# Performance work log

Hardware: AMD Instinct MI355X
Metric: run time of the kernel (lower is better)

## Reference

```python
import jax, jax.numpy as jnp
import numpy as np
import math

B, C_IN, N_SEL, N_DROP, HEADS = 4, 128, 1024, 1024, 4
Q_OUT = K_OUT = V_OUT = 256
N = N_SEL + N_DROP


def setup_inputs() -> dict:
    key = jax.random.key(0)
    ks = jax.random.split(key, 8)
    pcd_up = jax.random.normal(ks[0], (B, C_IN, N), jnp.float32)
    points_select = jax.random.normal(ks[1], (B, C_IN, N_SEL), jnp.float32)
    points_drop = jax.random.normal(ks[2], (B, C_IN, N_DROP), jnp.float32)
    # per-batch permutation of [0, N) split into select/drop halves (collision-free scatter)
    perms = jax.vmap(lambda k: jax.random.permutation(k, N))(jax.random.split(ks[3], B))
    idx_select = perms[:, None, :N_SEL].astype(jnp.int32)
    idx_drop = perms[:, None, N_SEL:].astype(jnp.int32)
    scale = 1.0 / math.sqrt(C_IN)
    Wq = jax.random.normal(ks[4], (Q_OUT, C_IN), jnp.float32) * scale
    Wk = jax.random.normal(ks[5], (K_OUT, C_IN), jnp.float32) * scale
    Wv = jax.random.normal(ks[6], (V_OUT, C_IN), jnp.float32) * scale
    Wskip = jax.random.normal(ks[7], (V_OUT, C_IN), jnp.float32) * scale
    return {"pcd_up": pcd_up, "points_select": points_select, "points_drop": points_drop,
            "idx_select": idx_select, "idx_drop": idx_drop,
            "Wq": Wq, "Wk": Wk, "Wv": Wv, "Wskip": Wskip}


def _concat_by_idx(a, b, idx_a, idx_b):
    # scatter columns of concat([a,b]) to positions given by concat([idx_a, idx_b])
    src = jnp.concatenate([a, b], axis=-1)            # (B, C, N)
    idx = jnp.concatenate([idx_a, idx_b], axis=-1)[:, 0, :]  # (B, N)
    return jax.vmap(lambda s, i: jnp.zeros_like(s).at[:, i].set(s))(src, idx)


def reference(pcd_up, points_select, points_drop, idx_select, idx_drop, Wq, Wk, Wv, Wskip):
    b, _, n = pcd_up.shape
    x = _concat_by_idx(points_select, points_drop, idx_select, idx_drop)  # (B, C_in, N)
    # 1x1 convs (no bias) == channel matmuls, then split heads: (B, H, D, N)
    q = jnp.einsum('oc,bcn->bon', Wq, x).reshape(b, HEADS, Q_OUT // HEADS, n)
    k = jnp.einsum('oc,bcn->bon', Wk, x).reshape(b, HEADS, K_OUT // HEADS, n)
    v = jnp.einsum('oc,bcn->bon', Wv, x).reshape(b, HEADS, V_OUT // HEADS, n)
    energy = jnp.einsum('bhdn,bhdm->bhnm', q, k)      # (B, H, N, N)
    attn = jax.nn.softmax(energy / math.sqrt(Q_OUT // HEADS), axis=-1)
    out = jnp.einsum('bhnm,bhdm->bhnd', attn, v)      # (B, H, N, Dv)
    out = out.transpose(0, 2, 1, 3).reshape(b, n, V_OUT).transpose(0, 2, 1)  # (B, V_out, N)
    skip = jnp.einsum('oc,bcn->bon', Wskip, pcd_up)   # (B, V_out, N)
    return skip + out
```

## Files before the change

### kernel.cpp

```cpp
#include <hip/hip_runtime.h>
#include <hip/hip_bf16.h>
#include <math.h>

#define B_    4
#define C_IN_ 128
#define N_    2048
#define NSEL_ 1024
#define H_    4
#define KS_   2

typedef __bf16 bf16;
typedef __bf16 bf16x2 __attribute__((ext_vector_type(2)));
typedef __bf16 bf16x4 __attribute__((ext_vector_type(4)));
typedef __bf16 bf16x8 __attribute__((ext_vector_type(8)));
typedef float  f32x4  __attribute__((ext_vector_type(4)));

__global__ __launch_bounds__(256) void prep_kernel(
    const int* __restrict__ isel, const int* __restrict__ idrp,
    const float* __restrict__ Wq, const float* __restrict__ Wk,
    const float* __restrict__ Wv, const float* __restrict__ Ws,
    int* __restrict__ inv, bf16* __restrict__ Wbf)
{
    const int blk = blockIdx.x;
    if (blk < 128) {
        int e = blk * 256 + threadIdx.x;
        int which = e >> 13, idx = e & 8191;
        const float* Wx = (which == 0) ? Wq : (which == 1) ? Wk
                        : (which == 2) ? Wv : Ws;
        float4 v = *(const float4*)(Wx + (size_t)idx * 4);
        bf16x4 o; o[0] = (bf16)v.x; o[1] = (bf16)v.y; o[2] = (bf16)v.z; o[3] = (bf16)v.w;
        *(bf16x4*)(Wbf + (size_t)which * 32768 + (size_t)idx * 4) = o;
    } else {
        int g = (blk - 128) * 256 + threadIdx.x;
        int b = g >> 11, j = g & (N_ - 1);
        int pos = (j < NSEL_) ? isel[b * NSEL_ + j] : idrp[b * NSEL_ + (j - NSEL_)];
        inv[b * N_ + (pos & (N_ - 1))] = j;
    }
}

#define XSTR 136

__global__ __launch_bounds__(256) void qkv_mfma_kernel(
    const float* __restrict__ pcd, const float* __restrict__ sel,
    const float* __restrict__ drop, const bf16* __restrict__ Wbf,
    bf16* __restrict__ qT, bf16* __restrict__ kTt, bf16* __restrict__ vTt)
{
    const int ntile = blockIdx.x;
    const int which = blockIdx.y >> 1;
    const int rh    = blockIdx.y & 1;
    const int b     = blockIdx.z;
    const int tid   = threadIdx.x;
    const int w     = tid >> 6;
    const int lane  = tid & 63;
    const int quad  = lane >> 4;
    const int lc    = lane & 15;
    const int n0    = ntile * 64;

    __shared__ __align__(16) bf16 xT[64 * XSTR];

    const float* srcp; int rstride;
    if (ntile < 16) { srcp = sel  + (size_t)b * C_IN_ * NSEL_ + n0;           rstride = NSEL_; }
    else            { srcp = drop + (size_t)b * C_IN_ * NSEL_ + (n0 - NSEL_); rstride = NSEL_; }

    #pragma unroll
    for (int k = 0; k < 4; ++k) {
        int e  = tid + k * 256;
        int cp = e >> 4, nq = e & 15;
        int c0 = cp * 2;
        float4 v0 = *(const float4*)(srcp + (size_t)c0 * rstride + nq * 4);
        float4 v1 = *(const float4*)(srcp + (size_t)(c0 + 1) * rstride + nq * 4);
        int cc = c0 ^ ((nq & 3) << 3);
        float a0[4] = {v0.x, v0.y, v0.z, v0.w};
        float a1[4] = {v1.x, v1.y, v1.z, v1.w};
        #pragma unroll
        for (int i = 0; i < 4; ++i) {
            int n = nq * 4 + i;
            bf16x2 t; t[0] = (bf16)a0[i]; t[1] = (bf16)a1[i];
            *(bf16x2*)&xT[n * XSTR + cc] = t;
        }
    }
    __syncthreads();

    const bf16* wbase = Wbf + (size_t)which * 256 * 128;
    const int rbase = rh * 128 + w * 32;

    f32x4 acc[8];
    #pragma unroll
    for (int i = 0; i < 8; ++i) acc[i] = (f32x4){0.f, 0.f, 0.f, 0.f};

    #pragma unroll
    for (int kq = 0; kq < 4; ++kq) {
        bf16x8 wf[2], xA[4];
        #pragma unroll
        for (int ot = 0; ot < 2; ++ot)
            wf[ot] = *(const bf16x8*)(wbase + (size_t)(rbase + ot * 16 + lc) * 128 + kq * 32 + quad * 8);
        #pragma unroll
        for (int nt = 0; nt < 4; ++nt) {
            int row = nt * 16 + lc;
            int col = (kq * 32 + quad * 8) ^ (((row >> 2) & 3) << 3);
            xA[nt] = *(const bf16x8*)&xT[row * XSTR + col];
        }
        if (which <= 1) {
            #pragma unroll
            for (int nt = 0; nt < 4; ++nt)
                #pragma unroll
                for (int ot = 0; ot < 2; ++ot)
                    acc[nt * 2 + ot] = __builtin_amdgcn_mfma_f32_16x16x32_bf16(xA[nt], wf[ot], acc[nt * 2 + ot], 0, 0, 0);
        } else {
            #pragma unroll
            for (int ot = 0; ot < 2; ++ot)
                #pragma unroll
                for (int nt = 0; nt < 4; ++nt)
                    acc[ot * 4 + nt] = __builtin_amdgcn_mfma_f32_16x16x32_bf16(wf[ot], xA[nt], acc[ot * 4 + nt], 0, 0, 0);
        }
    }

    if (which <= 1) {
        #pragma unroll
        for (int nt = 0; nt < 4; ++nt) {
            #pragma unroll
            for (int ot = 0; ot < 2; ++ot) {
                #pragma unroll
                for (int r = 0; r < 4; ++r) {
                    int n    = n0 + nt * 16 + quad * 4 + r;
                    int rloc = nt * 16 + quad * 4 + r;
                    int o256 = rbase + ot * 16 + lc;
                    int h = o256 >> 6, d = o256 & 63;
                    float val = acc[nt * 2 + ot][r];
                    if (which == 0)
                        qT[((size_t)(b * H_ + h) * N_ + n) * 64 + d] = (bf16)(val * 0.125f);
                    else
                        kTt[(((size_t)(b * H_ + h) * 32 + ntile) << 12) | (rloc << 6) | d] = (bf16)val;
                }
            }
        }
    } else {
        #pragma unroll
        for (int ot = 0; ot < 2; ++ot) {
            #pragma unroll
            for (int r = 0; r < 4; ++r) {
                int o256 = rbase + ot * 16 + quad * 4 + r;
                int h = o256 >> 6, dv = o256 & 63;
                bf16x4 pk;
                #pragma unroll
                for (int nt = 0; nt < 4; ++nt) pk[nt] = (bf16)acc[ot * 4 + nt][r];
                *(bf16x4*)(vTt + ((((size_t)(b * H_ + h) * 32 + ntile) << 12) | (dv << 6) | (lc * 4))) = pk;
            }
        }
    }
}

#define PSTR 72
#define KVSTR 72

__global__ __launch_bounds__(256, 2) void attn_kernel(
    const bf16* __restrict__ qT, const bf16* __restrict__ kTt,
    const bf16* __restrict__ vTt, bf16* __restrict__ Opart,
    float* __restrict__ S_ws)
{
    const int id    = blockIdx.x;
    const int bh    = (id & 7) + 8 * ((id >> 3) & 1);
    const int qb    = (id >> 4) & 15;
    const int c     = id >> 8;
    const int b     = bh >> 2;
    const int h     = bh & 3;
    const int tid   = threadIdx.x;
    const int w     = tid >> 6;
    const int lane  = tid & 63;
    const int quad  = lane >> 4;
    const int lc    = lane & 15;
    const int n0    = qb * 128 + w * 32;

    __shared__ __align__(16) bf16 sK[2][64 * KVSTR];
    __shared__ __align__(16) bf16 sV[2][64 * KVSTR];
    __shared__ __align__(16) bf16 p_lds[4 * 16 * PSTR];
    bf16* pw = &p_lds[w * 16 * PSTR];

    bf16x8 aq[2][2];
    #pragma unroll
    for (int t = 0; t < 2; ++t) {
        const bf16* qp = qT + ((size_t)bh * N_ + n0 + t * 16 + lc) * 64 + quad * 8;
        aq[t][0] = *(const bf16x8*)(qp);
        aq[t][1] = *(const bf16x8*)(qp + 32);
    }

    const bf16* kbase = kTt + (((size_t)bh * 32 + c * 16) << 12);
    const bf16* vbase = vTt + (((size_t)bh * 32 + c * 16) << 12);

    const int l0 = (tid >> 3) * KVSTR + (tid & 7) * 8;
    const int l1 = ((tid >> 3) + 32) * KVSTR + (tid & 7) * 8;

    bf16x8 ldK0 = *(const bf16x8*)(kbase + tid * 8);
    bf16x8 ldK1 = *(const bf16x8*)(kbase + 2048 + tid * 8);
    bf16x8 ldV0 = *(const bf16x8*)(vbase + tid * 8);
    bf16x8 ldV1 = *(const bf16x8*)(vbase + 2048 + tid * 8);

    f32x4 accO[2][4];
    #pragma unroll
    for (int t = 0; t < 2; ++t)
        #pragma unroll
        for (int i = 0; i < 4; ++i) accO[t][i] = (f32x4){0.f, 0.f, 0.f, 0.f};
    float psum[2][4] = {{0.f,0.f,0.f,0.f},{0.f,0.f,0.f,0.f}};

    for (int s = 0; s < 16; ++s) {
        const int buf = s & 1;
        *(bf16x8*)&sK[buf][l0] = ldK0;
        *(bf16x8*)&sK[buf][l1] = ldK1;
        *(bf16x8*)&sV[buf][l0] = ldV0;
        *(bf16x8*)&sV[buf][l1] = ldV1;
        __syncthreads();

        if (s < 15) {
            const bf16* kg = kbase + ((size_t)(s + 1) << 12);
            const bf16* vg = vbase + ((size_t)(s + 1) << 12);
            ldK0 = *(const bf16x8*)(kg + tid * 8);
            ldK1 = *(const bf16x8*)(kg + 2048 + tid * 8);
            ldV0 = *(const bf16x8*)(vg + tid * 8);
            ldV1 = *(const bf16x8*)(vg + 2048 + tid * 8);
        }

        bf16x8 kf[4][2], vf[4][2];
        #pragma unroll
        for (int mt = 0; mt < 4; ++mt) {
            const int rb = (mt * 16 + lc) * KVSTR + quad * 8;
            kf[mt][0] = *(const bf16x8*)&sK[buf][rb];
            kf[mt][1] = *(const bf16x8*)&sK[buf][rb + 32];
            vf[mt][0] = *(const bf16x8*)&sV[buf][rb];
            vf[mt][1] = *(const bf16x8*)&sV[buf][rb + 32];
        }

        #pragma unroll
        for (int t = 0; t < 2; ++t) {
            f32x4 accS[4];
            #pragma unroll
            for (int mt = 0; mt < 4; ++mt) {
                f32x4 z = (f32x4){0.f, 0.f, 0.f, 0.f};
                z = __builtin_amdgcn_mfma_f32_16x16x32_bf16(aq[t][0], kf[mt][0], z, 0, 0, 0);
                z = __builtin_amdgcn_mfma_f32_16x16x32_bf16(aq[t][1], kf[mt][1], z, 0, 0, 0);
                accS[mt] = z;
            }
            #pragma unroll
            for (int r = 0; r < 4; ++r) {
                float sum = 0.f;
                #pragma unroll
                for (int mt = 0; mt < 4; ++mt) {
                    float p = __expf(accS[mt][r]);
                    accS[mt][r] = p;
                    sum += p;
                }
                psum[t][r] += sum;
            }
            #pragma unroll
            for (int r = 0; r < 4; ++r) {
                bf16x4 pk;
                #pragma unroll
                for (int mt = 0; mt < 4; ++mt) pk[mt] = (bf16)accS[mt][r];
                *(bf16x4*)&pw[(quad * 4 + r) * PSTR + lc * 4] = pk;
            }
            bf16x8 ap0 = *(const bf16x8*)(&pw[lc * PSTR + quad * 8]);
            bf16x8 ap1 = *(const bf16x8*)(&pw[lc * PSTR + 32 + quad * 8]);
            #pragma unroll
            for (int dvt = 0; dvt < 4; ++dvt) {
                accO[t][dvt] = __builtin_amdgcn_mfma_f32_16x16x32_bf16(ap0, vf[dvt][0], accO[t][dvt], 0, 0, 0);
                accO[t][dvt] = __builtin_amdgcn_mfma_f32_16x16x32_bf16(ap1, vf[dvt][1], accO[t][dvt], 0, 0, 0);
            }
        }
    }

    #pragma unroll
    for (int t = 0; t < 2; ++t) {
        float inv[4];
        #pragma unroll
        for (int r = 0; r < 4; ++r) {
            float s = psum[t][r];
            #pragma unroll
            for (int off = 1; off < 16; off <<= 1)
                s += __shfl_xor(s, off, 64);
            inv[r] = 1.f / s;
            int n = n0 + t * 16 + quad * 4 + r;
            if (lc == 0)
                S_ws[((size_t)(c * B_ + b) * H_ + h) * N_ + n] = s;
        }
        #pragma unroll
        for (int r = 0; r < 4; ++r) {
            int n = n0 + t * 16 + quad * 4 + r;
            #pragma unroll
            for (int dvt = 0; dvt < 4; ++dvt) {
                int o = h * 64 + dvt * 16 + lc;
                Opart[((size_t)(c * B_ + b) * N_ + n) * 256 + o] = (bf16)(accO[t][dvt][r] * inv[r]);
            }
        }
    }
}

__global__ __launch_bounds__(256) void scatter_kernel(
    const bf16* __restrict__ Opart, const float* __restrict__ S_ws,
    const int* __restrict__ inv, const float* __restrict__ pcd,
    const bf16* __restrict__ Wbf, float* __restrict__ out)
{
    const int ptile = blockIdx.x;
    const int og    = blockIdx.y;
    const int b     = blockIdx.z;
    const int tid   = threadIdx.x;
    const int w     = tid >> 6;
    const int lane  = tid & 63;
    const int quad  = lane >> 4;
    const int lc    = lane & 15;
    const int p0    = ptile * 64;

    __shared__ __align__(16) bf16 xT[64 * XSTR];
    __shared__ __align__(16) bf16 lds[64 * 72];
    __shared__ float wls[KS_][64];
    __shared__ int   jrow[64];

    const float* srcp = pcd + (size_t)b * C_IN_ * N_ + p0;
    #pragma unroll
    for (int k = 0; k < 4; ++k) {
        int e  = tid + k * 256;
        int cp = e >> 4, nq = e & 15;
        int c0 = cp * 2;
        float4 v0 = *(const float4*)(srcp + (size_t)c0 * N_ + nq * 4);
        float4 v1 = *(const float4*)(srcp + (size_t)(c0 + 1) * N_ + nq * 4);
        int cc = c0 ^ ((nq & 3) << 3);
        float a0[4] = {v0.x, v0.y, v0.z, v0.w};
        float a1[4] = {v1.x, v1.y, v1.z, v1.w};
        #pragma unroll
        for (int i = 0; i < 4; ++i) {
            int n = nq * 4 + i;
            bf16x2 t; t[0] = (bf16)a0[i]; t[1] = (bf16)a1[i];
            *(bf16x2*)&xT[n * XSTR + cc] = t;
        }
    }
    if (tid < 64) {
        int row = tid;
        int j = inv[b * N_ + p0 + row] & (N_ - 1);
        jrow[row] = j;
        float sv[KS_]; float denom = 0.f;
        #pragma unroll
        for (int c = 0; c < KS_; ++c) {
            sv[c] = S_ws[((size_t)(c * B_ + b) * H_ + og) * N_ + j];
            denom += sv[c];
        }
        float idn = 1.f / denom;
        #pragma unroll
        for (int c = 0; c < KS_; ++c) wls[c][row] = sv[c] * idn;
    }
    __syncthreads();

    const bf16* wbase = Wbf + (size_t)3 * 256 * 128 + (size_t)(og * 64 + w * 16) * 128;
    f32x4 acc[4];
    #pragma unroll
    for (int i = 0; i < 4; ++i) acc[i] = (f32x4){0.f, 0.f, 0.f, 0.f};
    #pragma unroll
    for (int kq = 0; kq < 4; ++kq) {
        bf16x8 A = *(const bf16x8*)(wbase + (size_t)lc * 128 + kq * 32 + quad * 8);
        #pragma unroll
        for (int nt = 0; nt < 4; ++nt) {
            int row = nt * 16 + lc;
            int col = (kq * 32 + quad * 8) ^ (((row >> 2) & 3) << 3);
            bf16x8 Bf = *(const bf16x8*)&xT[row * XSTR + col];
            acc[nt] = __builtin_amdgcn_mfma_f32_16x16x32_bf16(A, Bf, acc[nt], 0, 0, 0);
        }
    }

    #pragma unroll
    for (int k = 0; k < 2; ++k) {
        int e = tid + k * 256;
        int row = e >> 3, seg = e & 7;
        int j = jrow[row];
        float a8[8];
        #pragma unroll
        for (int i = 0; i < 8; ++i) a8[i] = 0.f;
        #pragma unroll
        for (int c = 0; c < KS_; ++c) {
            bf16x8 v = *(const bf16x8*)(Opart + ((size_t)(c * B_ + b) * N_ + j) * 256 + og * 64 + seg * 8);
            float wgt = wls[c][row];
            #pragma unroll
            for (int i = 0; i < 8; ++i) a8[i] += wgt * (float)v[i];
        }
        bf16x8 o8;
        #pragma unroll
        for (int i = 0; i < 8; ++i) o8[i] = (bf16)a8[i];
        *(bf16x8*)&lds[row * 72 + seg * 8] = o8;
    }
    __syncthreads();

    #pragma unroll
    for (int nt = 0; nt < 4; ++nt) {
        #pragma unroll
        for (int r = 0; r < 4; ++r) {
            int o_loc = w * 16 + quad * 4 + r;
            int p     = nt * 16 + lc;
            float attn = (float)lds[p * 72 + o_loc];
            out[((size_t)b * 256 + og * 64 + o_loc) * N_ + p0 + p] = acc[nt][r] + attn;
        }
    }
}

extern "C" void kernel_launch(void* const* d_in, const int* in_sizes, int n_in,
                              void* d_out, int out_size, void* d_ws, size_t ws_size,
                              hipStream_t stream) {
    const float* pcd  = (const float*)d_in[0];
    const float* sel  = (const float*)d_in[1];
    const float* drop = (const float*)d_in[2];
    const int*   isel = (const int*)d_in[3];
    const int*   idrp = (const int*)d_in[4];
    const float* Wq   = (const float*)d_in[5];
    const float* Wk   = (const float*)d_in[6];
    const float* Wv   = (const float*)d_in[7];
    const float* Ws   = (const float*)d_in[8];
    float* out = (float*)d_out;

    const size_t MB = 1024 * 1024;
    char*  ws    = (char*)d_ws;
    bf16*  qT    = (bf16*)(ws);
    bf16*  kTt   = (bf16*)(ws + 4 * MB);
    bf16*  vTt   = (bf16*)(ws + 8 * MB);
    bf16*  Opart = (bf16*)(ws + 12 * MB);
    float* S_ws  = (float*)(ws + 20 * MB);
    bf16*  Wbf   = (bf16*)(ws + 20 * MB + 256 * 1024);
    int*   inv   = (int*)(ws + 20 * MB + 512 * 1024);

    prep_kernel<<<dim3(160), 256, 0, stream>>>(isel, idrp, Wq, Wk, Wv, Ws, inv, Wbf);
    qkv_mfma_kernel<<<dim3(32, 6, B_), 256, 0, stream>>>(pcd, sel, drop, Wbf,
                                                         qT, kTt, vTt);
    attn_kernel<<<dim3(16 * 16 * KS_), 256, 0, stream>>>(qT, kTt, vTt, Opart, S_ws);
    scatter_kernel<<<dim3(32, 4, B_), 256, 0, stream>>>(Opart, S_ws, inv, pcd, Wbf, out);
}
```

Baseline: 117.9 us.

## Fuse prep into QKV, use direct global-to-LDS loads and exp2 softmax in attention

Removes the separate prep kernel: weights are converted from fp32 to bf16 on the fly inside the GEMM kernels, and the inverse-permutation scatter is folded into the QKV kernel. The attention kernel now loads K/V tiles straight into LDS with global_load_lds using an XOR-swizzled layout (written that way by the QKV kernel) instead of staging through registers and a padded stride. It also folds log2(e) into the Q scale so the softmax can use exp2, raises the occupancy hint to 3 blocks per SIMD, and adds setprio around the MFMA blocks. The scatter kernel issues its gathers earlier for latency hiding. The cost is redundant weight conversion per block and a dependency on the swizzle agreeing across both kernels.

```diff
diff --git a/kernel.cpp b/kernel.cpp
--- a/kernel.cpp
+++ b/kernel.cpp
@@ -15,34 +15,27 @@
 typedef __bf16 bf16x8 __attribute__((ext_vector_type(8)));
 typedef float  f32x4  __attribute__((ext_vector_type(4)));
 
-__global__ __launch_bounds__(256) void prep_kernel(
+__device__ __forceinline__ void gll16(const void* g, void* l) {
+    __builtin_amdgcn_global_load_lds((const __attribute__((address_space(1))) void*)g,
+                                     (__attribute__((address_space(3))) void*)l,
+                                     16, 0, 0);
+}
+
+__device__ __forceinline__ bf16x8 cvt8(float4 a, float4 b) {
+    bf16x8 r;
+    r[0] = (bf16)a.x; r[1] = (bf16)a.y; r[2] = (bf16)a.z; r[3] = (bf16)a.w;
+    r[4] = (bf16)b.x; r[5] = (bf16)b.y; r[6] = (bf16)b.z; r[7] = (bf16)b.w;
+    return r;
+}
+
+#define XSTR 136
+
+__global__ __launch_bounds__(256) void qkv_mfma_kernel(
+    const float* __restrict__ sel, const float* __restrict__ drop,
+    const float* __restrict__ Wq, const float* __restrict__ Wk,
+    const float* __restrict__ Wv,
     const int* __restrict__ isel, const int* __restrict__ idrp,
-    const float* __restrict__ Wq, const float* __restrict__ Wk,
-    const float* __restrict__ Wv, const float* __restrict__ Ws,
-    int* __restrict__ inv, bf16* __restrict__ Wbf)
-{
-    const int blk = blockIdx.x;
-    if (blk < 128) {
-        int e = blk * 256 + threadIdx.x;
-        int which = e >> 13, idx = e & 8191;
-        const float* Wx = (which == 0) ? Wq : (which == 1) ? Wk
-                        : (which == 2) ? Wv : Ws;
-        float4 v = *(const float4*)(Wx + (size_t)idx * 4);
-        bf16x4 o; o[0] = (bf16)v.x; o[1] = (bf16)v.y; o[2] = (bf16)v.z; o[3] = (bf16)v.w;
-        *(bf16x4*)(Wbf + (size_t)which * 32768 + (size_t)idx * 4) = o;
-    } else {
-        int g = (blk - 128) * 256 + threadIdx.x;
-        int b = g >> 11, j = g & (N_ - 1);
-        int pos = (j < NSEL_) ? isel[b * NSEL_ + j] : idrp[b * NSEL_ + (j - NSEL_)];
-        inv[b * N_ + (pos & (N_ - 1))] = j;
-    }
-}
-
-#define XSTR 136
-
-__global__ __launch_bounds__(256) void qkv_mfma_kernel(
-    const float* __restrict__ pcd, const float* __restrict__ sel,
-    const float* __restrict__ drop, const bf16* __restrict__ Wbf,
+    int* __restrict__ inv,
     bf16* __restrict__ qT, bf16* __restrict__ kTt, bf16* __restrict__ vTt)
 {
     const int ntile = blockIdx.x;
@@ -58,6 +51,12 @@
 
     __shared__ __align__(16) bf16 xT[64 * XSTR];
 
+    if (blockIdx.y == 0 && ntile < 8) {
+        int j = ntile * 256 + tid;
+        int pos = (j < NSEL_) ? isel[b * NSEL_ + j] : idrp[b * NSEL_ + (j - NSEL_)];
+        inv[b * N_ + (pos & (N_ - 1))] = j;
+    }
+
     const float* srcp; int rstride;
     if (ntile < 16) { srcp = sel  + (size_t)b * C_IN_ * NSEL_ + n0;           rstride = NSEL_; }
     else            { srcp = drop + (size_t)b * C_IN_ * NSEL_ + (n0 - NSEL_); rstride = NSEL_; }
@@ -81,7 +80,7 @@
     }
     __syncthreads();
 
-    const bf16* wbase = Wbf + (size_t)which * 256 * 128;
+    const float* Wx = (which == 0) ? Wq : (which == 1) ? Wk : Wv;
     const int rbase = rh * 128 + w * 32;
 
     f32x4 acc[8];
@@ -92,8 +91,12 @@
     for (int kq = 0; kq < 4; ++kq) {
         bf16x8 wf[2], xA[4];
         #pragma unroll
-        for (int ot = 0; ot < 2; ++ot)
-            wf[ot] = *(const bf16x8*)(wbase + (size_t)(rbase + ot * 16 + lc) * 128 + kq * 32 + quad * 8);
+        for (int ot = 0; ot < 2; ++ot) {
+            const float* wp = Wx + (size_t)(rbase + ot * 16 + lc) * 128 + kq * 32 + quad * 8;
+            float4 u0 = *(const float4*)wp;
+            float4 u1 = *(const float4*)(wp + 4);
+            wf[ot] = cvt8(u0, u1);
+        }
         #pragma unroll
         for (int nt = 0; nt < 4; ++nt) {
             int row = nt * 16 + lc;
@@ -128,9 +131,9 @@
                     int h = o256 >> 6, d = o256 & 63;
                     float val = acc[nt * 2 + ot][r];
                     if (which == 0)
-                        qT[((size_t)(b * H_ + h) * N_ + n) * 64 + d] = (bf16)(val * 0.125f);
+                        qT[((size_t)(b * H_ + h) * N_ + n) * 64 + d] = (bf16)(val * 0.18033688011f);
                     else
-                        kTt[(((size_t)(b * H_ + h) * 32 + ntile) << 12) | (rloc << 6) | d] = (bf16)val;
+                        kTt[(((size_t)(b * H_ + h) * 32 + ntile) << 12) | (rloc << 6) | (d ^ ((rloc & 7) << 3))] = (bf16)val;
                 }
             }
         }
@@ -144,16 +147,16 @@
                 bf16x4 pk;
                 #pragma unroll
                 for (int nt = 0; nt < 4; ++nt) pk[nt] = (bf16)acc[ot * 4 + nt][r];
-                *(bf16x4*)(vTt + ((((size_t)(b * H_ + h) * 32 + ntile) << 12) | (dv << 6) | (lc * 4))) = pk;
+                int scol = (lc * 4) ^ ((dv & 7) << 3);
+                *(bf16x4*)(vTt + ((((size_t)(b * H_ + h) * 32 + ntile) << 12) | (dv << 6) | scol)) = pk;
             }
         }
     }
 }
 
 #define PSTR 72
-#define KVSTR 72
-
-__global__ __launch_bounds__(256, 2) void attn_kernel(
+
+__global__ __launch_bounds__(256, 3) void attn_kernel(
     const bf16* __restrict__ qT, const bf16* __restrict__ kTt,
     const bf16* __restrict__ vTt, bf16* __restrict__ Opart,
     float* __restrict__ S_ws)
@@ -171,10 +174,20 @@
     const int lc    = lane & 15;
     const int n0    = qb * 128 + w * 32;
 
-    __shared__ __align__(16) bf16 sK[2][64 * KVSTR];
-    __shared__ __align__(16) bf16 sV[2][64 * KVSTR];
+    __shared__ __align__(16) bf16 sK[2][64 * 64];
+    __shared__ __align__(16) bf16 sV[2][64 * 64];
     __shared__ __align__(16) bf16 p_lds[4 * 16 * PSTR];
     bf16* pw = &p_lds[w * 16 * PSTR];
+
+    const bf16* kbase = kTt + (((size_t)bh * 32 + c * 16) << 12);
+    const bf16* vbase = vTt + (((size_t)bh * 32 + c * 16) << 12);
+
+    #pragma unroll
+    for (int j = 0; j < 2; ++j) {
+        const int sseg = (w * 2 + j) << 9;
+        gll16(kbase + sseg + lane * 8, &sK[0][sseg]);
+        gll16(vbase + sseg + lane * 8, &sV[0][sseg]);
+    }
 
     bf16x8 aq[2][2];
     #pragma unroll
@@ -184,17 +197,6 @@
         aq[t][1] = *(const bf16x8*)(qp + 32);
     }
 
-    const bf16* kbase = kTt + (((size_t)bh * 32 + c * 16) << 12);
-    const bf16* vbase = vTt + (((size_t)bh * 32 + c * 16) << 12);
-
-    const int l0 = (tid >> 3) * KVSTR + (tid & 7) * 8;
-    const int l1 = ((tid >> 3) + 32) * KVSTR + (tid & 7) * 8;
-
-    bf16x8 ldK0 = *(const bf16x8*)(kbase + tid * 8);
-    bf16x8 ldK1 = *(const bf16x8*)(kbase + 2048 + tid * 8);
-    bf16x8 ldV0 = *(const bf16x8*)(vbase + tid * 8);
-    bf16x8 ldV1 = *(const bf16x8*)(vbase + 2048 + tid * 8);
-
     f32x4 accO[2][4];
     #pragma unroll
     for (int t = 0; t < 2; ++t)
@@ -202,36 +204,37 @@
         for (int i = 0; i < 4; ++i) accO[t][i] = (f32x4){0.f, 0.f, 0.f, 0.f};
     float psum[2][4] = {{0.f,0.f,0.f,0.f},{0.f,0.f,0.f,0.f}};
 
+    const int rswz = (lc & 7) << 3;
+
     for (int s = 0; s < 16; ++s) {
         const int buf = s & 1;
-        *(bf16x8*)&sK[buf][l0] = ldK0;
-        *(bf16x8*)&sK[buf][l1] = ldK1;
-        *(bf16x8*)&sV[buf][l0] = ldV0;
-        *(bf16x8*)&sV[buf][l1] = ldV1;
         __syncthreads();
 
         if (s < 15) {
             const bf16* kg = kbase + ((size_t)(s + 1) << 12);
             const bf16* vg = vbase + ((size_t)(s + 1) << 12);
-            ldK0 = *(const bf16x8*)(kg + tid * 8);
-            ldK1 = *(const bf16x8*)(kg + 2048 + tid * 8);
-            ldV0 = *(const bf16x8*)(vg + tid * 8);
-            ldV1 = *(const bf16x8*)(vg + 2048 + tid * 8);
+            #pragma unroll
+            for (int j = 0; j < 2; ++j) {
+                const int sseg = (w * 2 + j) << 9;
+                gll16(kg + sseg + lane * 8, &sK[buf ^ 1][sseg]);
+                gll16(vg + sseg + lane * 8, &sV[buf ^ 1][sseg]);
+            }
         }
 
         bf16x8 kf[4][2], vf[4][2];
         #pragma unroll
         for (int mt = 0; mt < 4; ++mt) {
-            const int rb = (mt * 16 + lc) * KVSTR + quad * 8;
-            kf[mt][0] = *(const bf16x8*)&sK[buf][rb];
-            kf[mt][1] = *(const bf16x8*)&sK[buf][rb + 32];
-            vf[mt][0] = *(const bf16x8*)&sV[buf][rb];
-            vf[mt][1] = *(const bf16x8*)&sV[buf][rb + 32];
+            const int rb = (mt * 16 + lc) * 64;
+            kf[mt][0] = *(const bf16x8*)&sK[buf][rb + ((quad * 8) ^ rswz)];
+            kf[mt][1] = *(const bf16x8*)&sK[buf][rb + ((quad * 8 + 32) ^ rswz)];
+            vf[mt][0] = *(const bf16x8*)&sV[buf][rb + ((quad * 8) ^ rswz)];
+            vf[mt][1] = *(const bf16x8*)&sV[buf][rb + ((quad * 8 + 32) ^ rswz)];
         }
 
         #pragma unroll
         for (int t = 0; t < 2; ++t) {
             f32x4 accS[4];
+            __builtin_amdgcn_s_setprio(1);
             #pragma unroll
             for (int mt = 0; mt < 4; ++mt) {
                 f32x4 z = (f32x4){0.f, 0.f, 0.f, 0.f};
@@ -239,12 +242,13 @@
                 z = __builtin_amdgcn_mfma_f32_16x16x32_bf16(aq[t][1], kf[mt][1], z, 0, 0, 0);
                 accS[mt] = z;
             }
+            __builtin_amdgcn_s_setprio(0);
             #pragma unroll
             for (int r = 0; r < 4; ++r) {
                 float sum = 0.f;
                 #pragma unroll
                 for (int mt = 0; mt < 4; ++mt) {
-                    float p = __expf(accS[mt][r]);
+                    float p = exp2f(accS[mt][r]);
                     accS[mt][r] = p;
                     sum += p;
                 }
@@ -259,24 +263,26 @@
             }
             bf16x8 ap0 = *(const bf16x8*)(&pw[lc * PSTR + quad * 8]);
             bf16x8 ap1 = *(const bf16x8*)(&pw[lc * PSTR + 32 + quad * 8]);
+            __builtin_amdgcn_s_setprio(1);
             #pragma unroll
             for (int dvt = 0; dvt < 4; ++dvt) {
                 accO[t][dvt] = __builtin_amdgcn_mfma_f32_16x16x32_bf16(ap0, vf[dvt][0], accO[t][dvt], 0, 0, 0);
                 accO[t][dvt] = __builtin_amdgcn_mfma_f32_16x16x32_bf16(ap1, vf[dvt][1], accO[t][dvt], 0, 0, 0);
             }
+            __builtin_amdgcn_s_setprio(0);
         }
     }
 
     #pragma unroll
     for (int t = 0; t < 2; ++t) {
-        float inv[4];
+        float inv_[4];
         #pragma unroll
         for (int r = 0; r < 4; ++r) {
             float s = psum[t][r];
             #pragma unroll
             for (int off = 1; off < 16; off <<= 1)
                 s += __shfl_xor(s, off, 64);
-            inv[r] = 1.f / s;
+            inv_[r] = 1.f / s;
             int n = n0 + t * 16 + quad * 4 + r;
             if (lc == 0)
                 S_ws[((size_t)(c * B_ + b) * H_ + h) * N_ + n] = s;
@@ -287,7 +293,7 @@
             #pragma unroll
             for (int dvt = 0; dvt < 4; ++dvt) {
                 int o = h * 64 + dvt * 16 + lc;
-                Opart[((size_t)(c * B_ + b) * N_ + n) * 256 + o] = (bf16)(accO[t][dvt][r] * inv[r]);
+                Opart[((size_t)(c * B_ + b) * N_ + n) * 256 + o] = (bf16)(accO[t][dvt][r] * inv_[r]);
             }
         }
     }
@@ -296,7 +302,7 @@
 __global__ __launch_bounds__(256) void scatter_kernel(
     const bf16* __restrict__ Opart, const float* __restrict__ S_ws,
     const int* __restrict__ inv, const float* __restrict__ pcd,
-    const bf16* __restrict__ Wbf, float* __restrict__ out)
+    const float* __restrict__ Ws, float* __restrict__ out)
 {
     const int ptile = blockIdx.x;
     const int og    = blockIdx.y;
@@ -310,8 +316,19 @@
 
     __shared__ __align__(16) bf16 xT[64 * XSTR];
     __shared__ __align__(16) bf16 lds[64 * 72];
-    __shared__ float wls[KS_][64];
-    __shared__ int   jrow[64];
+
+    const int row0 = tid >> 3, seg = tid & 7, row1 = row0 + 32;
+    int j0 = inv[b * N_ + p0 + row0] & (N_ - 1);
+    int j1 = inv[b * N_ + p0 + row1] & (N_ - 1);
+    float sv0[KS_], sv1[KS_];
+    bf16x8 g0[KS_], g1[KS_];
+    #pragma unroll
+    for (int cc = 0; cc < KS_; ++cc) {
+        g0[cc] = *(const bf16x8*)(Opart + (((size_t)(cc * B_ + b) * N_ + j0) << 8) + og * 64 + seg * 8);
+        g1[cc] = *(const bf16x8*)(Opart + (((size_t)(cc * B_ + b) * N_ + j1) << 8) + og * 64 + seg * 8);
+        sv0[cc] = S_ws[((size_t)(cc * B_ + b) * H_ + og) * N_ + j0];
+        sv1[cc] = S_ws[((size_t)(cc * B_ + b) * H_ + og) * N_ + j1];
+    }
 
     const float* srcp = pcd + (size_t)b * C_IN_ * N_ + p0;
     #pragma unroll
@@ -331,29 +348,17 @@
             *(bf16x2*)&xT[n * XSTR + cc] = t;
         }
     }
-    if (tid < 64) {
-        int row = tid;
-        int j = inv[b * N_ + p0 + row] & (N_ - 1);
-        jrow[row] = j;
-        float sv[KS_]; float denom = 0.f;
-        #pragma unroll
-        for (int c = 0; c < KS_; ++c) {
-            sv[c] = S_ws[((size_t)(c * B_ + b) * H_ + og) * N_ + j];
-            denom += sv[c];
-        }
-        float idn = 1.f / denom;
-        #pragma unroll
-        for (int c = 0; c < KS_; ++c) wls[c][row] = sv[c] * idn;
-    }
     __syncthreads();
 
-    const bf16* wbase = Wbf + (size_t)3 * 256 * 128 + (size_t)(og * 64 + w * 16) * 128;
     f32x4 acc[4];
     #pragma unroll
     for (int i = 0; i < 4; ++i) acc[i] = (f32x4){0.f, 0.f, 0.f, 0.f};
     #pragma unroll
     for (int kq = 0; kq < 4; ++kq) {
-        bf16x8 A = *(const bf16x8*)(wbase + (size_t)lc * 128 + kq * 32 + quad * 8);
+        const float* wp = Ws + (size_t)(og * 64 + w * 16 + lc) * 128 + kq * 32 + quad * 8;
+        float4 u0 = *(const float4*)wp;
+        float4 u1 = *(const float4*)(wp + 4);
+        bf16x8 A = cvt8(u0, u1);
         #pragma unroll
         for (int nt = 0; nt < 4; ++nt) {
             int row = nt * 16 + lc;
@@ -363,25 +368,28 @@
         }
     }
 
-    #pragma unroll
-    for (int k = 0; k < 2; ++k) {
-        int e = tid + k * 256;
-        int row = e >> 3, seg = e & 7;
-        int j = jrow[row];
-        float a8[8];
-        #pragma unroll
-        for (int i = 0; i < 8; ++i) a8[i] = 0.f;
-        #pragma unroll
-        for (int c = 0; c < KS_; ++c) {
-            bf16x8 v = *(const bf16x8*)(Opart + ((size_t)(c * B_ + b) * N_ + j) * 256 + og * 64 + seg * 8);
-            float wgt = wls[c][row];
-            #pragma unroll
-            for (int i = 0; i < 8; ++i) a8[i] += wgt * (float)v[i];
-        }
-        bf16x8 o8;
-        #pragma unroll
-        for (int i = 0; i < 8; ++i) o8[i] = (bf16)a8[i];
-        *(bf16x8*)&lds[row * 72 + seg * 8] = o8;
+    {
+        float d0 = 0.f, d1 = 0.f;
+        #pragma unroll
+        for (int cc = 0; cc < KS_; ++cc) { d0 += sv0[cc]; d1 += sv1[cc]; }
+        float id0 = 1.f / d0, id1 = 1.f / d1;
+        float a8[8], b8[8];
+        #pragma unroll
+        for (int i = 0; i < 8; ++i) { a8[i] = 0.f; b8[i] = 0.f; }
+        #pragma unroll
+        for (int cc = 0; cc < KS_; ++cc) {
+            float w0 = sv0[cc] * id0, w1 = sv1[cc] * id1;
+            #pragma unroll
+            for (int i = 0; i < 8; ++i) {
+                a8[i] += w0 * (float)g0[cc][i];
+                b8[i] += w1 * (float)g1[cc][i];
+            }
+        }
+        bf16x8 o8, p8;
+        #pragma unroll
+        for (int i = 0; i < 8; ++i) { o8[i] = (bf16)a8[i]; p8[i] = (bf16)b8[i]; }
+        *(bf16x8*)&lds[row0 * 72 + seg * 8] = o8;
+        *(bf16x8*)&lds[row1 * 72 + seg * 8] = p8;
     }
     __syncthreads();
 
@@ -418,12 +426,11 @@
     bf16*  vTt   = (bf16*)(ws + 8 * MB);
     bf16*  Opart = (bf16*)(ws + 12 * MB);
     float* S_ws  = (float*)(ws + 20 * MB);
-    bf16*  Wbf   = (bf16*)(ws + 20 * MB + 256 * 1024);
-    int*   inv   = (int*)(ws + 20 * MB + 512 * 1024);
-
-    prep_kernel<<<dim3(160), 256, 0, stream>>>(isel, idrp, Wq, Wk, Wv, Ws, inv, Wbf);
-    qkv_mfma_kernel<<<dim3(32, 6, B_), 256, 0, stream>>>(pcd, sel, drop, Wbf,
+    int*   inv   = (int*)(ws + 20 * MB + 256 * 1024);
+
+    qkv_mfma_kernel<<<dim3(32, 6, B_), 256, 0, stream>>>(sel, drop, Wq, Wk, Wv,
+                                                         isel, idrp, inv,
                                                          qT, kTt, vTt);
     attn_kernel<<<dim3(16 * 16 * KS_), 256, 0, stream>>>(qT, kTt, vTt, Opart, S_ws);
-    scatter_kernel<<<dim3(32, 4, B_), 256, 0, stream>>>(Opart, S_ws, inv, pcd, Wbf, out);
-}
+    scatter_kernel<<<dim3(32, 4, B_), 256, 0, stream>>>(Opart, S_ws, inv, pcd, Ws, out);
+}
```

Measured after the change: 126.3 us. +7.2%, slower.
